# Performance work log

Hardware: AMD Instinct MI355X
Metric: run time of the kernel (lower is better)

## Reference

```python
import jax, jax.numpy as jnp
import numpy as np

N_NODES = 100000
N_EDGES = 1600000
D_IN = 128
D_HID = 128
D_OUT = 32


def setup_inputs() -> dict:
    key = jax.random.key(0)
    ks = jax.random.split(key, 10)
    x = jax.random.normal(ks[0], (N_NODES, D_IN), dtype=jnp.float32)
    edge_index = jax.random.randint(ks[1], (2, N_EDGES), 0, N_NODES, dtype=jnp.int64)
    s = 0.05
    return {
        "x": x,
        "edge_index": edge_index,
        "Wl0": jax.random.normal(ks[2], (D_IN, D_HID), jnp.float32) * s,
        "bl0": jnp.zeros((D_HID,), jnp.float32),
        "Wr0": jax.random.normal(ks[3], (D_IN, D_HID), jnp.float32) * s,
        "Wl1": jax.random.normal(ks[4], (D_HID, D_HID), jnp.float32) * s,
        "bl1": jnp.zeros((D_HID,), jnp.float32),
        "Wr1": jax.random.normal(ks[5], (D_HID, D_HID), jnp.float32) * s,
        "Wl2": jax.random.normal(ks[6], (D_HID, D_OUT), jnp.float32) * s,
        "bl2": jnp.zeros((D_OUT,), jnp.float32),
        "Wr2": jax.random.normal(ks[7], (D_HID, D_OUT), jnp.float32) * s,
    }


def _sage_conv(x, src, dst, Wl, bl, Wr):
    # PyG SAGEConv (aggr='mean', root_weight=True):
    # out[i] = lin_l(mean_{j in N(i)} x_j) + lin_r(x_i)
    n = x.shape[0]
    msgs = x[src]                                        # [E, F] gather
    agg = jax.ops.segment_sum(msgs, dst, num_segments=n) # [N, F] scatter-add
    deg = jax.ops.segment_sum(jnp.ones((src.shape[0],), x.dtype), dst, num_segments=n)
    mean = agg / jnp.maximum(deg, 1.0)[:, None]
    return mean @ Wl + bl + x @ Wr


def reference(x, edge_index, Wl0, bl0, Wr0, Wl1, bl1, Wr1, Wl2, bl2, Wr2):
    src, dst = edge_index[0], edge_index[1]
    h = jax.nn.relu(_sage_conv(x, src, dst, Wl0, bl0, Wr0))
    h = jax.nn.relu(_sage_conv(h, src, dst, Wl1, bl1, Wr1))
    h = _sage_conv(h, src, dst, Wl2, bl2, Wr2)
    return jax.nn.log_softmax(h, axis=1)
```

## Files before the change

### kernel.cpp

```cpp
#include <hip/hip_runtime.h>
#include <hip/hip_bf16.h>
#include <math.h>

#define NN 100000
#define NE 1600000

#define NCB 391
#define EB  8192
#define SCT 512
#define HBK 128

typedef __attribute__((ext_vector_type(8))) short short8;
typedef __attribute__((ext_vector_type(4))) float f32x4;

__device__ __forceinline__ unsigned short f2bf(float f) {
  union { float f; unsigned int i; } v; v.f = f;
  unsigned int i = v.i;
  unsigned int r = (i + 0x7FFFu + ((i >> 16) & 1u)) >> 16;
  return (unsigned short)r;
}
__device__ __forceinline__ float bflo(unsigned int u) {
  union { unsigned int i; float f; } v; v.i = u << 16; return v.f;
}
__device__ __forceinline__ float bfhi(unsigned int u) {
  union { unsigned int i; float f; } v; v.i = u & 0xFFFF0000u; return v.f;
}
__device__ __forceinline__ float bf1(unsigned short u) {
  union { unsigned int i; float f; } v; v.i = ((unsigned int)u) << 16; return v.f;
}

__global__ __launch_bounds__(512) void k_chist(const int* __restrict__ dst,
                                               int* __restrict__ part) {
  __shared__ int h[NCB];
  for (int i = threadIdx.x; i < NCB; i += 512) h[i] = 0;
  __syncthreads();
  int stride = HBK * 512;
  for (int e = blockIdx.x * 512 + threadIdx.x; e < NE; e += stride) {
    int d = dst[e];
    d = d < 0 ? 0 : (d >= NN ? NN - 1 : d);
    atomicAdd(&h[d >> 8], 1);
  }
  __syncthreads();
  for (int i = threadIdx.x; i < NCB; i += 512) part[blockIdx.x * NCB + i] = h[i];
}

__global__ __launch_bounds__(512) void k_cscan(const int* __restrict__ part,
                                               int* __restrict__ cboff,
                                               int* __restrict__ ccur,
                                               int* __restrict__ csroff) {
  __shared__ int sd[512];
  int t = threadIdx.x;
  int v = 0;
  if (t < NCB) {
    int s0 = 0, s1 = 0, s2 = 0, s3 = 0;
    #pragma unroll 4
    for (int k = 0; k < HBK; k += 4) {
      s0 += part[(k + 0) * NCB + t];
      s1 += part[(k + 1) * NCB + t];
      s2 += part[(k + 2) * NCB + t];
      s3 += part[(k + 3) * NCB + t];
    }
    v = (s0 + s1) + (s2 + s3);
    ccur[t] = 0;
  }
  sd[t] = v;
  __syncthreads();
  for (int st = 1; st < 512; st <<= 1) {
    int x = (t >= st) ? sd[t - st] : 0;
    __syncthreads();
    sd[t] += x;
    __syncthreads();
  }
  if (t < NCB) cboff[t] = sd[t] - v;
  if (t == NCB - 1) { cboff[NCB] = sd[t]; csroff[NN] = sd[t]; }
}

__global__ __launch_bounds__(SCT) void k_cscatter(
    const int* __restrict__ src, const int* __restrict__ dst,
    const int* __restrict__ cboff, int* __restrict__ ccur,
    unsigned int* __restrict__ ebuf) {
  __shared__ int lh[NCB];
  __shared__ unsigned int sRank[EB];
  __shared__ unsigned int sPay[EB];
  int t = threadIdx.x;
  int base = blockIdx.x * EB;
  for (int i = t; i < NCB; i += SCT) lh[i] = 0;
  __syncthreads();
  #pragma unroll
  for (int i = 0; i < EB / SCT; i++) {
    int idx = i * SCT + t;
    int e = base + idx;
    unsigned int rk = 0xFFFFFFFFu, pv = 0;
    if (e < NE) {
      int d = dst[e];
      d = d < 0 ? 0 : (d >= NN ? NN - 1 : d);
      int s = src[e];
      s = s < 0 ? 0 : (s >= NN ? NN - 1 : s);
      int cb = d >> 8;
      int r = atomicAdd(&lh[cb], 1);
      rk = (((unsigned int)cb) << 13) | (unsigned int)r;
      pv = (((unsigned int)(d & 255)) << 17) | (unsigned int)s;
    }
    sRank[idx] = rk;
    sPay[idx]  = pv;
  }
  __syncthreads();
  for (int i = t; i < NCB; i += SCT) {
    int c = lh[i];
    int g = c ? atomicAdd(&ccur[i], c) : 0;
    lh[i] = cboff[i] + g;
  }
  __syncthreads();
  #pragma unroll
  for (int i = 0; i < EB / SCT; i++) {
    int idx = i * SCT + t;
    unsigned int rk = sRank[idx];
    if (rk != 0xFFFFFFFFu) {
      int cb = rk >> 13;
      int r  = rk & 0x1FFF;
      ebuf[lh[cb] + r] = sPay[idx];
    }
  }
}

__global__ __launch_bounds__(256) void k_crefine(
    const unsigned int* __restrict__ ebuf, const int* __restrict__ cboff,
    int* __restrict__ csroff, float* __restrict__ invd,
    int* __restrict__ csrsrc) {
  __shared__ int lh[256], pos[256], cur[256];
  int b = blockIdx.x, t = threadIdx.x;
  lh[t] = 0; cur[t] = 0;
  __syncthreads();
  int beg = cboff[b], end = cboff[b + 1];
  for (int i = beg + t; i < end; i += 256) atomicAdd(&lh[ebuf[i] >> 17], 1);
  __syncthreads();
  int v = lh[t];
  pos[t] = v;
  __syncthreads();
  for (int st = 1; st < 256; st <<= 1) {
    int x = (t >= st) ? pos[t - st] : 0;
    __syncthreads();
    pos[t] += x;
    __syncthreads();
  }
  int nid = b * 256 + t;
  int mybase = cboff[b] + pos[t] - v;
  if (nid < NN) {
    csroff[nid] = mybase;
    invd[nid] = 1.0f / (float)(v < 1 ? 1 : v);
  }
  __syncthreads();
  pos[t] = mybase;
  __syncthreads();
  for (int i = beg + t; i < end; i += 256) {
    unsigned int u = ebuf[i];
    int local = u >> 17;
    int r = atomicAdd(&cur[local], 1);
    csrsrc[pos[local] + r] = (int)(u & 0x1FFFFu);
  }
}

__global__ void k_wprep(const float* __restrict__ Wl0, const float* __restrict__ Wr0,
                        const float* __restrict__ Wl1, const float* __restrict__ Wr1,
                        const float* __restrict__ Wl2, const float* __restrict__ Wr2,
                        unsigned short* __restrict__ B0,
                        unsigned short* __restrict__ B1,
                        unsigned short* __restrict__ B2) {
  int idx = blockIdx.x * 256 + threadIdx.x;
  if (idx < 32768) {
    int n = idx >> 7, k = idx & 127;
    float v = (n < 128) ? Wl0[k * 128 + n] : Wr0[k * 128 + (n - 128)];
    B0[idx] = f2bf(v);
  } else if (idx < 65536) {
    int j = idx - 32768;
    int n = j >> 7, k = j & 127;
    float v = (n < 128) ? Wl1[k * 128 + n] : Wr1[k * 128 + (n - 128)];
    B1[j] = f2bf(v);
  } else if (idx < 73728) {
    int j = idx - 65536;
    int n = j >> 7, k = j & 127;
    float v = (n < 32) ? Wl2[k * 32 + n] : Wr2[k * 32 + (n - 32)];
    B2[j] = f2bf(v);
  }
}

template <int NC, int AFP32>
__global__ __launch_bounds__(512) void k_mgemm(
    const void* __restrict__ Ap, const unsigned short* __restrict__ Bp,
    const float* __restrict__ bias,
    unsigned short* __restrict__ yl, unsigned short* __restrict__ yr) {
  __shared__ unsigned short sA[128 * 136];
  int tid = threadIdx.x;
  int nb  = blockIdx.x * 128;

  if (AFP32) {
    const float* A = (const float*)Ap;
    #pragma unroll
    for (int i = 0; i < 8; i++) {
      int j = i * 512 + tid;
      int m = j >> 5;
      int k4 = (j & 31) * 4;
      int gn = nb + m;
      float4 v = make_float4(0.f, 0.f, 0.f, 0.f);
      if (gn < NN) v = *(const float4*)&A[gn * 128 + k4];
      unsigned int p0 = (unsigned int)f2bf(v.x) | ((unsigned int)f2bf(v.y) << 16);
      unsigned int p1 = (unsigned int)f2bf(v.z) | ((unsigned int)f2bf(v.w) << 16);
      *(uint2*)&sA[m * 136 + k4] = make_uint2(p0, p1);
    }
  } else {
    const unsigned short* A = (const unsigned short*)Ap;
    #pragma unroll
    for (int i = 0; i < 4; i++) {
      int j = i * 512 + tid;
      int m = j >> 4;
      int k8 = (j & 15) * 8;
      int gn = nb + m;
      uint4 v = make_uint4(0, 0, 0, 0);
      if (gn < NN) v = *(const uint4*)&A[gn * 128 + k8];
      *(uint4*)&sA[m * 136 + k8] = v;
    }
  }
  __syncthreads();

  int wave = tid >> 6, lane = tid & 63;
  int l15 = lane & 15, lq = lane >> 4;
  constexpr int MT = (NC == 256) ? 4 : 2;
  constexpr int NT = (NC == 256) ? 4 : 2;
  int wm, wn;
  if (NC == 256) { wm = wave & 1; wn = wave >> 1; }
  else           { wm = wave >> 1; wn = wave & 1; }
  int mbase = wm * (MT * 16);
  int nbase = wn * (NT * 16);

  f32x4 acc[MT][NT];
  #pragma unroll
  for (int mi = 0; mi < MT; mi++)
    #pragma unroll
    for (int ni = 0; ni < NT; ni++) acc[mi][ni] = (f32x4){0.f, 0.f, 0.f, 0.f};

  #pragma unroll
  for (int kc = 0; kc < 4; kc++) {
    int k0 = kc * 32 + lq * 8;
    short8 af[MT], bfr[NT];
    #pragma unroll
    for (int ni = 0; ni < NT; ni++)
      bfr[ni] = *(const short8*)&Bp[(nbase + ni * 16 + l15) * 128 + k0];
    #pragma unroll
    for (int mi = 0; mi < MT; mi++)
      af[mi] = *(const short8*)&sA[(mbase + mi * 16 + l15) * 136 + k0];
    #pragma unroll
    for (int mi = 0; mi < MT; mi++)
      #pragma unroll
      for (int ni = 0; ni < NT; ni++)
        acc[mi][ni] = __builtin_amdgcn_mfma_f32_16x16x32_bf16(
            af[mi], bfr[ni], acc[mi][ni], 0, 0, 0);
  }

  constexpr int HC = NC / 2;
  #pragma unroll
  for (int mi = 0; mi < MT; mi++) {
    #pragma unroll
    for (int ni = 0; ni < NT; ni++) {
      int n = nbase + ni * 16 + l15;
      #pragma unroll
      for (int r = 0; r < 4; r++) {
        int gn = nb + mbase + mi * 16 + lq * 4 + r;
        if (gn < NN) {
          float v = acc[mi][ni][r];
          if (n < HC) {
            yl[(size_t)gn * HC + n] = f2bf(v);
          } else {
            int n2 = n - HC;
            yr[(size_t)gn * HC + n2] = f2bf(v + bias[n2]);
          }
        }
      }
    }
  }
}

__global__ __launch_bounds__(256) void k_agg128(
    const unsigned short* __restrict__ yl, const unsigned short* __restrict__ yr,
    const int* __restrict__ off, const int* __restrict__ csr,
    const float* __restrict__ invd, unsigned short* __restrict__ out, int relu) {
  int wid  = (blockIdx.x * 256 + threadIdx.x) >> 6;
  int lane = threadIdx.x & 63;
  if (wid >= NN) return;
  int beg = off[wid], end = off[wid + 1];
  const unsigned int* ylp = (const unsigned int*)yl;
  float ax0 = 0.f, ay0 = 0.f, ax1 = 0.f, ay1 = 0.f;
  float ax2 = 0.f, ay2 = 0.f, ax3 = 0.f, ay3 = 0.f;
  int e = beg;
  for (; e + 7 < end; e += 8) {
    int s0 = csr[e],     s1 = csr[e + 1], s2 = csr[e + 2], s3 = csr[e + 3];
    int s4 = csr[e + 4], s5 = csr[e + 5], s6 = csr[e + 6], s7 = csr[e + 7];
    unsigned int u0 = ylp[s0 * 64 + lane];
    unsigned int u1 = ylp[s1 * 64 + lane];
    unsigned int u2 = ylp[s2 * 64 + lane];
    unsigned int u3 = ylp[s3 * 64 + lane];
    unsigned int u4 = ylp[s4 * 64 + lane];
    unsigned int u5 = ylp[s5 * 64 + lane];
    unsigned int u6 = ylp[s6 * 64 + lane];
    unsigned int u7 = ylp[s7 * 64 + lane];
    ax0 += bflo(u0); ay0 += bfhi(u0);
    ax1 += bflo(u1); ay1 += bfhi(u1);
    ax2 += bflo(u2); ay2 += bfhi(u2);
    ax3 += bflo(u3); ay3 += bfhi(u3);
    ax0 += bflo(u4); ay0 += bfhi(u4);
    ax1 += bflo(u5); ay1 += bfhi(u5);
    ax2 += bflo(u6); ay2 += bfhi(u6);
    ax3 += bflo(u7); ay3 += bfhi(u7);
  }
  for (; e < end; e++) {
    int s = csr[e];
    unsigned int u = ylp[s * 64 + lane];
    ax0 += bflo(u); ay0 += bfhi(u);
  }
  float sc = invd[wid];
  unsigned int rv = ((const unsigned int*)yr)[wid * 64 + lane];
  float vx = ((ax0 + ax1) + (ax2 + ax3)) * sc + bflo(rv);
  float vy = ((ay0 + ay1) + (ay2 + ay3)) * sc + bfhi(rv);
  if (relu) { vx = fmaxf(vx, 0.f); vy = fmaxf(vy, 0.f); }
  ((unsigned int*)out)[wid * 64 + lane] =
      (unsigned int)f2bf(vx) | ((unsigned int)f2bf(vy) << 16);
}

__global__ __launch_bounds__(256) void k_agg32_lsm(
    const unsigned short* __restrict__ yl, const unsigned short* __restrict__ yr,
    const int* __restrict__ off, const int* __restrict__ csr,
    const float* __restrict__ invd, float* __restrict__ out) {
  int row  = (blockIdx.x * 256 + threadIdx.x) >> 5;
  int lane = threadIdx.x & 31;
  if (row >= NN) return;
  int beg = off[row], end = off[row + 1];
  float a0 = 0.f, a1 = 0.f, a2 = 0.f, a3 = 0.f;
  int e = beg;
  for (; e + 3 < end; e += 4) {
    int s0 = csr[e], s1 = csr[e + 1], s2 = csr[e + 2], s3 = csr[e + 3];
    a0 += bf1(yl[s0 * 32 + lane]);
    a1 += bf1(yl[s1 * 32 + lane]);
    a2 += bf1(yl[s2 * 32 + lane]);
    a3 += bf1(yl[s3 * 32 + lane]);
  }
  for (; e < end; e++) a0 += bf1(yl[csr[e] * 32 + lane]);
  float v = ((a0 + a1) + (a2 + a3)) * invd[row] + bf1(yr[row * 32 + lane]);
  float m = v;
  #pragma unroll
  for (int o = 16; o; o >>= 1) m = fmaxf(m, __shfl_xor(m, o, 32));
  float ex = expf(v - m);
  float s = ex;
  #pragma unroll
  for (int o = 16; o; o >>= 1) s += __shfl_xor(s, o, 32);
  out[row * 32 + lane] = v - m - logf(s);
}


extern "C" void kernel_launch(void* const* d_in, const int* in_sizes, int n_in,
                              void* d_out, int out_size, void* d_ws, size_t ws_size,
                              hipStream_t stream) {
  (void)in_sizes; (void)n_in; (void)out_size; (void)ws_size;
  const float* x   = (const float*)d_in[0];
  const int*   ei  = (const int*)d_in[1];
  const float* Wl0 = (const float*)d_in[2];
  const float* bl0 = (const float*)d_in[3];
  const float* Wr0 = (const float*)d_in[4];
  const float* Wl1 = (const float*)d_in[5];
  const float* bl1 = (const float*)d_in[6];
  const float* Wr1 = (const float*)d_in[7];
  const float* Wl2 = (const float*)d_in[8];
  const float* bl2 = (const float*)d_in[9];
  const float* Wr2 = (const float*)d_in[10];
  const int* srcI = ei;
  const int* dstI = ei + NE;

  char* w = (char*)d_ws;
  int*   ccur   = (int*)(w + (16 << 10));
  int*   cboff  = (int*)(w + (32 << 10));
  unsigned short* B0 = (unsigned short*)(w + (64 << 10));
  unsigned short* B1 = (unsigned short*)(w + (160 << 10));
  unsigned short* B2 = (unsigned short*)(w + (256 << 10));
  int*   part   = (int*)(w + (288 << 10));
  int*   csroff = (int*)(w + (512 << 10));
  float* invd   = (float*)(w + (1024 << 10));
  unsigned int* ebuf = (unsigned int*)(w + (size_t)(2) * 1024 * 1024);
  int*   csrsrc = (int*)(w + (size_t)(9) * 1024 * 1024);
  unsigned short* ylb = (unsigned short*)(w + (size_t)(16) * 1024 * 1024);
  unsigned short* yrb = (unsigned short*)(w + (size_t)(48) * 1024 * 1024);
  unsigned short* hb  = (unsigned short*)(w + (size_t)(80) * 1024 * 1024);

  k_chist<<<HBK, 512, 0, stream>>>(dstI, part);
  k_cscan<<<1, 512, 0, stream>>>(part, cboff, ccur, csroff);
  k_cscatter<<<(NE + EB - 1) / EB, SCT, 0, stream>>>(srcI, dstI, cboff, ccur, ebuf);
  k_crefine<<<NCB, 256, 0, stream>>>(ebuf, cboff, csroff, invd, csrsrc);

  k_wprep<<<(73728 + 255) / 256, 256, 0, stream>>>(Wl0, Wr0, Wl1, Wr1, Wl2, Wr2,
                                                   B0, B1, B2);

  dim3 gg((NN + 127) / 128);
  k_mgemm<256, 1><<<gg, 512, 0, stream>>>(x, B0, bl0, ylb, yrb);
  k_agg128<<<(NN * 64) / 256, 256, 0, stream>>>(ylb, yrb, csroff, csrsrc, invd, hb, 1);
  k_mgemm<256, 0><<<gg, 512, 0, stream>>>(hb, B1, bl1, ylb, yrb);
  k_agg128<<<(NN * 64) / 256, 256, 0, stream>>>(ylb, yrb, csroff, csrsrc, invd, hb, 1);
  k_mgemm<64, 0><<<gg, 512, 0, stream>>>(hb, B2, bl2, ylb, yrb);
  k_agg32_lsm<<<(NN * 32) / 256, 256, 0, stream>>>(ylb, yrb, csroff, csrsrc, invd,
                                                   (float*)d_out);
}
```

Measured before the change: 461.1 us.

## Merge histogram with weight prep and scatter with first GEMM into shared launches

Merges the dst histogram with bf16 weight conversion into one launch, and runs the edge-scatter blocks and the layer-0 GEMM blocks inside one kernel, dispatched by block index. The goal is to cut launch count and let the independent CSR build and first-layer GEMM overlap on the GPU. The histogram block count is also halved. As a cost, the combined kernel reserves the larger scatter shared-memory footprint (about 66KB) for every block, which can lower occupancy for the GEMM blocks.

```diff
diff --git a/kernel.cpp b/kernel.cpp
--- a/kernel.cpp
+++ b/kernel.cpp
@@ -8,7 +8,9 @@
 #define NCB 391
 #define EB  8192
 #define SCT 512
-#define HBK 128
+#define HBK 64
+#define NSB 196
+#define WPB 144
 
 typedef __attribute__((ext_vector_type(8))) short short8;
 typedef __attribute__((ext_vector_type(4))) float f32x4;
@@ -29,19 +31,43 @@
   union { unsigned int i; float f; } v; v.i = ((unsigned int)u) << 16; return v.f;
 }
 
-__global__ __launch_bounds__(512) void k_chist(const int* __restrict__ dst,
-                                               int* __restrict__ part) {
-  __shared__ int h[NCB];
-  for (int i = threadIdx.x; i < NCB; i += 512) h[i] = 0;
-  __syncthreads();
-  int stride = HBK * 512;
-  for (int e = blockIdx.x * 512 + threadIdx.x; e < NE; e += stride) {
-    int d = dst[e];
-    d = d < 0 ? 0 : (d >= NN ? NN - 1 : d);
-    atomicAdd(&h[d >> 8], 1);
-  }
-  __syncthreads();
-  for (int i = threadIdx.x; i < NCB; i += 512) part[blockIdx.x * NCB + i] = h[i];
+__global__ __launch_bounds__(512) void k_prep(
+    const int* __restrict__ dst, int* __restrict__ part,
+    const float* __restrict__ Wl0, const float* __restrict__ Wr0,
+    const float* __restrict__ Wl1, const float* __restrict__ Wr1,
+    const float* __restrict__ Wl2, const float* __restrict__ Wr2,
+    unsigned short* __restrict__ B0, unsigned short* __restrict__ B1,
+    unsigned short* __restrict__ B2) {
+  if (blockIdx.x < HBK) {
+    __shared__ int h[NCB];
+    for (int i = threadIdx.x; i < NCB; i += 512) h[i] = 0;
+    __syncthreads();
+    int stride = HBK * 512;
+    for (int e = blockIdx.x * 512 + threadIdx.x; e < NE; e += stride) {
+      int d = dst[e];
+      d = d < 0 ? 0 : (d >= NN ? NN - 1 : d);
+      atomicAdd(&h[d >> 8], 1);
+    }
+    __syncthreads();
+    for (int i = threadIdx.x; i < NCB; i += 512) part[blockIdx.x * NCB + i] = h[i];
+  } else {
+    int idx = (blockIdx.x - HBK) * 512 + threadIdx.x;
+    if (idx < 32768) {
+      int n = idx >> 7, k = idx & 127;
+      float v = (n < 128) ? Wl0[k * 128 + n] : Wr0[k * 128 + (n - 128)];
+      B0[idx] = f2bf(v);
+    } else if (idx < 65536) {
+      int j = idx - 32768;
+      int n = j >> 7, k = j & 127;
+      float v = (n < 128) ? Wl1[k * 128 + n] : Wr1[k * 128 + (n - 128)];
+      B1[j] = f2bf(v);
+    } else if (idx < 73728) {
+      int j = idx - 65536;
+      int n = j >> 7, k = j & 127;
+      float v = (n < 32) ? Wl2[k * 32 + n] : Wr2[k * 32 + (n - 32)];
+      B2[j] = f2bf(v);
+    }
+  }
 }
 
 __global__ __launch_bounds__(512) void k_cscan(const int* __restrict__ part,
@@ -75,15 +101,17 @@
   if (t == NCB - 1) { cboff[NCB] = sd[t]; csroff[NN] = sd[t]; }
 }
 
-__global__ __launch_bounds__(SCT) void k_cscatter(
+
+__device__ __forceinline__ void cscatter_body(
+    char* smem, int bid,
     const int* __restrict__ src, const int* __restrict__ dst,
     const int* __restrict__ cboff, int* __restrict__ ccur,
     unsigned int* __restrict__ ebuf) {
-  __shared__ int lh[NCB];
-  __shared__ unsigned int sRank[EB];
-  __shared__ unsigned int sPay[EB];
+  int* lh = (int*)smem;
+  unsigned int* sRank = (unsigned int*)(smem + 1600);
+  unsigned int* sPay  = (unsigned int*)(smem + 1600 + EB * 4);
   int t = threadIdx.x;
-  int base = blockIdx.x * EB;
+  int base = bid * EB;
   for (int i = t; i < NCB; i += SCT) lh[i] = 0;
   __syncthreads();
   #pragma unroll
@@ -123,6 +151,95 @@
   }
 }
 
+__device__ __forceinline__ void mgemm0_body(
+    char* smem, int bid, const float* __restrict__ A,
+    const unsigned short* __restrict__ Bp, const float* __restrict__ bias,
+    unsigned short* __restrict__ yl, unsigned short* __restrict__ yr) {
+  unsigned short* sA = (unsigned short*)smem;
+  int tid = threadIdx.x;
+  int nb  = bid * 128;
+
+  #pragma unroll
+  for (int i = 0; i < 8; i++) {
+    int j = i * 512 + tid;
+    int m = j >> 5;
+    int k4 = (j & 31) * 4;
+    int gn = nb + m;
+    float4 v = make_float4(0.f, 0.f, 0.f, 0.f);
+    if (gn < NN) v = *(const float4*)&A[gn * 128 + k4];
+    unsigned int p0 = (unsigned int)f2bf(v.x) | ((unsigned int)f2bf(v.y) << 16);
+    unsigned int p1 = (unsigned int)f2bf(v.z) | ((unsigned int)f2bf(v.w) << 16);
+    *(uint2*)&sA[m * 136 + k4] = make_uint2(p0, p1);
+  }
+  __syncthreads();
+
+  int wave = tid >> 6, lane = tid & 63;
+  int l15 = lane & 15, lq = lane >> 4;
+  int wm = wave & 1, wn = wave >> 1;
+  int mbase = wm * 64;
+  int nbase = wn * 64;
+
+  f32x4 acc[4][4];
+  #pragma unroll
+  for (int mi = 0; mi < 4; mi++)
+    #pragma unroll
+    for (int ni = 0; ni < 4; ni++) acc[mi][ni] = (f32x4){0.f, 0.f, 0.f, 0.f};
+
+  #pragma unroll
+  for (int kc = 0; kc < 4; kc++) {
+    int k0 = kc * 32 + lq * 8;
+    short8 af[4], bfr[4];
+    #pragma unroll
+    for (int ni = 0; ni < 4; ni++)
+      bfr[ni] = *(const short8*)&Bp[(nbase + ni * 16 + l15) * 128 + k0];
+    #pragma unroll
+    for (int mi = 0; mi < 4; mi++)
+      af[mi] = *(const short8*)&sA[(mbase + mi * 16 + l15) * 136 + k0];
+    #pragma unroll
+    for (int mi = 0; mi < 4; mi++)
+      #pragma unroll
+      for (int ni = 0; ni < 4; ni++)
+        acc[mi][ni] = __builtin_amdgcn_mfma_f32_16x16x32_bf16(
+            af[mi], bfr[ni], acc[mi][ni], 0, 0, 0);
+  }
+
+  #pragma unroll
+  for (int mi = 0; mi < 4; mi++) {
+    #pragma unroll
+    for (int ni = 0; ni < 4; ni++) {
+      int n = nbase + ni * 16 + l15;
+      #pragma unroll
+      for (int r = 0; r < 4; r++) {
+        int gn = nb + mbase + mi * 16 + lq * 4 + r;
+        if (gn < NN) {
+          float v = acc[mi][ni][r];
+          if (n < 128) {
+            yl[(size_t)gn * 128 + n] = f2bf(v);
+          } else {
+            int n2 = n - 128;
+            yr[(size_t)gn * 128 + n2] = f2bf(v + bias[n2]);
+          }
+        }
+      }
+    }
+  }
+}
+
+__global__ __launch_bounds__(512) void k_scatgemm(
+    const int* __restrict__ src, const int* __restrict__ dst,
+    const int* __restrict__ cboff, int* __restrict__ ccur,
+    unsigned int* __restrict__ ebuf,
+    const float* __restrict__ x, const unsigned short* __restrict__ B0,
+    const float* __restrict__ bias,
+    unsigned short* __restrict__ yl, unsigned short* __restrict__ yr) {
+  __shared__ char smem[1600 + EB * 8];
+  if (blockIdx.x < NSB) {
+    cscatter_body(smem, blockIdx.x, src, dst, cboff, ccur, ebuf);
+  } else {
+    mgemm0_body(smem, blockIdx.x - NSB, x, B0, bias, yl, yr);
+  }
+}
+
 __global__ __launch_bounds__(256) void k_crefine(
     const unsigned int* __restrict__ ebuf, const int* __restrict__ cboff,
     int* __restrict__ csroff, float* __restrict__ invd,
@@ -160,65 +277,24 @@
   }
 }
 
-__global__ void k_wprep(const float* __restrict__ Wl0, const float* __restrict__ Wr0,
-                        const float* __restrict__ Wl1, const float* __restrict__ Wr1,
-                        const float* __restrict__ Wl2, const float* __restrict__ Wr2,
-                        unsigned short* __restrict__ B0,
-                        unsigned short* __restrict__ B1,
-                        unsigned short* __restrict__ B2) {
-  int idx = blockIdx.x * 256 + threadIdx.x;
-  if (idx < 32768) {
-    int n = idx >> 7, k = idx & 127;
-    float v = (n < 128) ? Wl0[k * 128 + n] : Wr0[k * 128 + (n - 128)];
-    B0[idx] = f2bf(v);
-  } else if (idx < 65536) {
-    int j = idx - 32768;
-    int n = j >> 7, k = j & 127;
-    float v = (n < 128) ? Wl1[k * 128 + n] : Wr1[k * 128 + (n - 128)];
-    B1[j] = f2bf(v);
-  } else if (idx < 73728) {
-    int j = idx - 65536;
-    int n = j >> 7, k = j & 127;
-    float v = (n < 32) ? Wl2[k * 32 + n] : Wr2[k * 32 + (n - 32)];
-    B2[j] = f2bf(v);
-  }
-}
-
-template <int NC, int AFP32>
+template <int NC>
 __global__ __launch_bounds__(512) void k_mgemm(
-    const void* __restrict__ Ap, const unsigned short* __restrict__ Bp,
+    const unsigned short* __restrict__ A, const unsigned short* __restrict__ Bp,
     const float* __restrict__ bias,
     unsigned short* __restrict__ yl, unsigned short* __restrict__ yr) {
   __shared__ unsigned short sA[128 * 136];
   int tid = threadIdx.x;
   int nb  = blockIdx.x * 128;
 
-  if (AFP32) {
-    const float* A = (const float*)Ap;
-    #pragma unroll
-    for (int i = 0; i < 8; i++) {
-      int j = i * 512 + tid;
-      int m = j >> 5;
-      int k4 = (j & 31) * 4;
-      int gn = nb + m;
-      float4 v = make_float4(0.f, 0.f, 0.f, 0.f);
-      if (gn < NN) v = *(const float4*)&A[gn * 128 + k4];
-      unsigned int p0 = (unsigned int)f2bf(v.x) | ((unsigned int)f2bf(v.y) << 16);
-      unsigned int p1 = (unsigned int)f2bf(v.z) | ((unsigned int)f2bf(v.w) << 16);
-      *(uint2*)&sA[m * 136 + k4] = make_uint2(p0, p1);
-    }
-  } else {
-    const unsigned short* A = (const unsigned short*)Ap;
-    #pragma unroll
-    for (int i = 0; i < 4; i++) {
-      int j = i * 512 + tid;
-      int m = j >> 4;
-      int k8 = (j & 15) * 8;
-      int gn = nb + m;
-      uint4 v = make_uint4(0, 0, 0, 0);
-      if (gn < NN) v = *(const uint4*)&A[gn * 128 + k8];
-      *(uint4*)&sA[m * 136 + k8] = v;
-    }
+  #pragma unroll
+  for (int i = 0; i < 4; i++) {
+    int j = i * 512 + tid;
+    int m = j >> 4;
+    int k8 = (j & 15) * 8;
+    int gn = nb + m;
+    uint4 v = make_uint4(0, 0, 0, 0);
+    if (gn < NN) v = *(const uint4*)&A[gn * 128 + k8];
+    *(uint4*)&sA[m * 136 + k8] = v;
   }
   __syncthreads();
 
@@ -388,20 +464,18 @@
   unsigned short* yrb = (unsigned short*)(w + (size_t)(48) * 1024 * 1024);
   unsigned short* hb  = (unsigned short*)(w + (size_t)(80) * 1024 * 1024);
 
-  k_chist<<<HBK, 512, 0, stream>>>(dstI, part);
+  dim3 gg((NN + 127) / 128);
+
+  k_prep<<<HBK + WPB, 512, 0, stream>>>(dstI, part, Wl0, Wr0, Wl1, Wr1, Wl2, Wr2,
+                                        B0, B1, B2);
   k_cscan<<<1, 512, 0, stream>>>(part, cboff, ccur, csroff);
-  k_cscatter<<<(NE + EB - 1) / EB, SCT, 0, stream>>>(srcI, dstI, cboff, ccur, ebuf);
+  k_scatgemm<<<NSB + 782, 512, 0, stream>>>(srcI, dstI, cboff, ccur, ebuf,
+                                            x, B0, bl0, ylb, yrb);
   k_crefine<<<NCB, 256, 0, stream>>>(ebuf, cboff, csroff, invd, csrsrc);
-
-  k_wprep<<<(73728 + 255) / 256, 256, 0, stream>>>(Wl0, Wr0, Wl1, Wr1, Wl2, Wr2,
-                                                   B0, B1, B2);
-
-  dim3 gg((NN + 127) / 128);
-  k_mgemm<256, 1><<<gg, 512, 0, stream>>>(x, B0, bl0, ylb, yrb);
   k_agg128<<<(NN * 64) / 256, 256, 0, stream>>>(ylb, yrb, csroff, csrsrc, invd, hb, 1);
-  k_mgemm<256, 0><<<gg, 512, 0, stream>>>(hb, B1, bl1, ylb, yrb);
+  k_mgemm<256><<<gg, 512, 0, stream>>>(hb, B1, bl1, ylb, yrb);
   k_agg128<<<(NN * 64) / 256, 256, 0, stream>>>(ylb, yrb, csroff, csrsrc, invd, hb, 1);
-  k_mgemm<64, 0><<<gg, 512, 0, stream>>>(hb, B2, bl2, ylb, yrb);
+  k_mgemm<64><<<gg, 512, 0, stream>>>(hb, B2, bl2, ylb, yrb);
   k_agg32_lsm<<<(NN * 32) / 256, 256, 0, stream>>>(ylb, yrb, csroff, csrsrc, invd,
                                                    (float*)d_out);
 }
```

New measurement: 450.7 us. 1.02x faster.
